# Kernel tuning notes

Measured on AMD Instinct MI355X. Metric: run time of the kernel, lower is better.

Reference implementation:

```python
import jax, jax.numpy as jnp
import numpy as np

N = 10000      # nodes
IN_DIM = 512   # input feature dim
HID = 512      # GCN hidden dim
OUT = 256      # embedding dim
E = 320000     # edges (avg degree 32)


def _normalize(x, eps=1e-12):
    # F.normalize: x / max(||x||_2, eps), row-wise
    n = jnp.sqrt(jnp.sum(x * x, axis=-1, keepdims=True))
    return x / jnp.maximum(n, eps)


def _gcn_conv(x, W, b, src, dst, n):
    # DGL GraphConv with norm='both': D_out^{-1/2} -> sum-aggregate -> D_in^{-1/2}, then bias
    ones = jnp.ones(src.shape[0], x.dtype)
    deg_out = jax.ops.segment_sum(ones, src, num_segments=n)
    deg_in = jax.ops.segment_sum(ones, dst, num_segments=n)
    ns = jnp.where(deg_out > 0, deg_out ** -0.5, 0.0)
    nd = jnp.where(deg_in > 0, deg_in ** -0.5, 0.0)
    h = x @ W                                  # weight first (math-equivalent)
    msg = h[src] * ns[src, None]               # gather + src-normalize
    agg = jax.ops.segment_sum(msg, dst, num_segments=n)  # scatter-sum to dst
    return agg * nd[:, None] + b


def _gcn(x, params, src, dst, n):
    W0, b0, W1, b1 = params
    h = jax.nn.relu(_gcn_conv(x, W0, b0, src, dst, n))
    return _gcn_conv(h, W1, b1, src, dst, n)


def _scores(v, u, Wp, bp, src, dst, n, tau):
    # pos_score: edge sim = <normalize(u)[src], normalize(proj(v))[dst]> / tau, scatter-mean to dst
    q = _normalize(v @ Wp + bp)
    un = _normalize(u)
    sim = jnp.sum(un[src] * q[dst], axis=1) / tau          # [E]
    cnt = jax.ops.segment_sum(jnp.ones_like(sim), dst, num_segments=n)
    denom = jnp.maximum(cnt, 1.0)                          # DGL mean gives 0 for deg-0 nodes
    pos = jax.ops.segment_sum(sim, dst, num_segments=n) / denom
    # neg_score: per-node total similarity (intra + inter), then per-edge log, scatter-mean
    z = _normalize(v)
    stu = _normalize(u)
    neg_sim = jnp.exp(z @ z.T / tau).sum(1) + jnp.exp(z @ stu.T / tau).sum(1)  # [N]
    m = jnp.log(neg_sim[dst] + jnp.exp(sim))               # udf_u_add_log_e
    neg = jax.ops.segment_sum(m, dst, num_segments=n) / denom
    return pos, neg


def setup_inputs() -> dict:
    key = jax.random.key(0)
    ks = jax.random.split(key, 16)
    feat = jax.random.normal(ks[0], (N, IN_DIM), jnp.float32)
    src_g = jax.random.randint(ks[1], (E,), 0, N)
    dst_g = jax.random.randint(ks[2], (E,), 0, N)
    src_s = jax.random.randint(ks[3], (E,), 0, N)
    dst_s = jax.random.randint(ks[4], (E,), 0, N)

    def lin(k, i, o, s=0.05):
        return jax.random.normal(k, (i, o), jnp.float32) * s

    inp = dict(
        feat=feat, src_g=src_g, dst_g=dst_g, src_s=src_s, dst_s=dst_s,
        tau1=jnp.ones((), jnp.float32), tau2=jnp.ones((), jnp.float32),
        # encoder1 (GCN, 2 layers) online + target (deepcopy -> independent params)
        W1a=lin(ks[5], IN_DIM, HID), b1a=jnp.zeros((HID,), jnp.float32),
        W1b=lin(ks[6], HID, OUT), b1b=jnp.zeros((OUT,), jnp.float32),
        W1a_t=lin(ks[7], IN_DIM, HID), b1a_t=jnp.zeros((HID,), jnp.float32),
        W1b_t=lin(ks[8], HID, OUT), b1b_t=jnp.zeros((OUT,), jnp.float32),
        # encoder2 (Linear) online + target
        W2=lin(ks[9], IN_DIM, OUT), b2=jnp.zeros((OUT,), jnp.float32),
        W2_t=lin(ks[10], IN_DIM, OUT), b2_t=jnp.zeros((OUT,), jnp.float32),
        # projector: Predictor(out, out, num_layers=1) -> single Linear
        Wp=lin(ks[11], OUT, OUT), bp=jnp.zeros((OUT,), jnp.float32),
    )
    return inp


def reference(feat, src_g, dst_g, src_s, dst_s, tau1, tau2,
              W1a, b1a, W1b, b1b, W1a_t, b1a_t, W1b_t, b1b_t,
              W2, b2, W2_t, b2_t, Wp, bp):
    n = feat.shape[0]
    # branch 1: GCN encoder
    v1 = _gcn(feat, (W1a, b1a, W1b, b1b), src_g, dst_g, n)
    u1 = _gcn(feat, (W1a_t, b1a_t, W1b_t, b1b_t), src_g, dst_g, n)
    pos1, neg1 = _scores(v1, u1, Wp, bp, src_s, dst_s, n, tau1)
    loss1 = jnp.mean(-pos1 + neg1)
    # branch 2: linear encoder
    v2 = feat @ W2 + b2
    u2 = feat @ W2_t + b2_t
    pos2, neg2 = _scores(v2, u2, Wp, bp, src_s, dst_s, n, tau2)
    loss2 = jnp.mean(-pos2 + neg2)
    return (v1, u1, v2, u2, loss1 + loss2)
```

## Files before the change

kernel.cpp:

```cpp
#include <hip/hip_runtime.h>

typedef __bf16 bf16x8 __attribute__((ext_vector_type(8)));
typedef float f32x4 __attribute__((ext_vector_type(4)));
typedef unsigned short u16x8 __attribute__((ext_vector_type(8)));

#define GLOAD16(gp, lp) __builtin_amdgcn_global_load_lds( \
    (const __attribute__((address_space(1))) void*)(gp), \
    (__attribute__((address_space(3))) void*)(lp), 16, 0, 0)

__device__ __forceinline__ unsigned short f2bf(float f) {
  union { float f; unsigned u; } c; c.f = f;
  unsigned u = c.u;
  u = (u + 0x7fffu + ((u >> 16) & 1u)) >> 16;
  return (unsigned short)u;
}
__device__ __forceinline__ float b2f(unsigned short u) {
  union { unsigned u; float f; } c; c.u = ((unsigned)u) << 16; return c.f;
}

__global__ void k_count(const int* __restrict__ src_g, const int* __restrict__ dst_g,
                        const int* __restrict__ dst_s,
                        int* deg_og, int* deg_ig, int* cnt_s, int E)
{
  int e = blockIdx.x * blockDim.x + threadIdx.x;
  if (e >= E) return;
  atomicAdd(&deg_og[src_g[e]], 1);
  atomicAdd(&deg_ig[dst_g[e]], 1);
  atomicAdd(&cnt_s[dst_s[e]], 1);
}

__global__ void k_norms(const int* __restrict__ deg_og, const int* __restrict__ deg_ig,
                        float* __restrict__ ns, float* __restrict__ nd, int N)
{
  int i = blockIdx.x * blockDim.x + threadIdx.x;
  if (i >= N) return;
  int a = deg_og[i]; ns[i] = a > 0 ? rsqrtf((float)a) : 0.f;
  int b = deg_ig[i]; nd[i] = b > 0 ? rsqrtf((float)b) : 0.f;
}

__global__ __launch_bounds__(1024) void k_scan(const int* __restrict__ deg0, int* __restrict__ offs0,
                                               const int* __restrict__ deg1, int* __restrict__ offs1, int N)
{
  const int* deg = blockIdx.x ? deg1 : deg0;
  int* offs = blockIdx.x ? offs1 : offs0;
  __shared__ int part[1024];
  const int t = threadIdx.x;
  const int CH = (N + 1023) / 1024;
  const int b = t * CH;
  int s = 0;
  for (int i = 0; i < CH; ++i) {
    int idx = b + i;
    s += (idx < N) ? deg[idx] : 0;
  }
  part[t] = s;
  __syncthreads();
  for (int o = 1; o < 1024; o <<= 1) {
    int v = (t >= o) ? part[t - o] : 0;
    __syncthreads();
    part[t] += v;
    __syncthreads();
  }
  int run = (t == 0) ? 0 : part[t - 1];
  if (t == 0) offs[0] = 0;
  for (int i = 0; i < CH; ++i) {
    int idx = b + i;
    if (idx < N) { run += deg[idx]; offs[idx + 1] = run; }
  }
}

__global__ void k_fill(const int* __restrict__ srcA, const int* __restrict__ dstA,
                       const int* __restrict__ offsA, int* curA, int* __restrict__ outA,
                       const int* __restrict__ srcB, const int* __restrict__ dstB,
                       const int* __restrict__ offsB, int* curB, int* __restrict__ outB, int E)
{
  int e = blockIdx.x * blockDim.x + threadIdx.x;
  if (e >= E) return;
  if (blockIdx.y == 0) {
    int d = dstA[e];
    int p = atomicAdd(&curA[d], 1);
    outA[offsA[d] + p] = srcA[e];
  } else {
    int d = dstB[e];
    int p = atomicAdd(&curB[d], 1);
    outB[offsB[d] + p] = srcB[e];
  }
}

struct PrepArgs {
  const float *feat, *W1a, *W1at, *W1b, *W1bt, *W2, *W2t, *Wp;
  const float *b1a, *b1at, *b1b, *b1bt, *b2, *b2t;
  unsigned short *featb, *wcatL1, *wcat2, *wcatLin, *wtp;
  float *bcatL1, *bcatGcn, *bcatLin;
  int NF;
};
__global__ void k_prep(PrepArgs p)
{
  int i = blockIdx.x * blockDim.x + threadIdx.x;
  if (i < p.NF) { p.featb[i] = f2bf(p.feat[i]); return; }
  i -= p.NF;
  if (i < 1024 * 512) {
    int n = i >> 9, k = i & 511;
    p.wcatL1[i] = f2bf(n < 512 ? p.W1a[k * 512 + n] : p.W1at[k * 512 + n - 512]);
    return;
  }
  i -= 1024 * 512;
  if (i < 512 * 512) {
    int n = i >> 9, k = i & 511;
    p.wcat2[i] = f2bf(n < 256 ? p.W1b[k * 256 + n] : p.W1bt[k * 256 + n - 256]);
    return;
  }
  i -= 512 * 512;
  if (i < 512 * 512) {
    int n = i >> 9, k = i & 511;
    p.wcatLin[i] = f2bf(n < 256 ? p.W2[k * 256 + n] : p.W2t[k * 256 + n - 256]);
    return;
  }
  i -= 512 * 512;
  if (i < 256 * 256) {
    int n = i >> 8, k = i & 255;
    p.wtp[i] = f2bf(p.Wp[k * 256 + n]);
    return;
  }
  i -= 256 * 256;
  if (i < 1024) { p.bcatL1[i] = i < 512 ? p.b1a[i] : p.b1at[i - 512]; return; }
  i -= 1024;
  if (i < 512) { p.bcatGcn[i] = i < 256 ? p.b1b[i] : p.b1bt[i - 256]; return; }
  i -= 512;
  if (i < 512) { p.bcatLin[i] = i < 256 ? p.b2[i] : p.b2t[i - 256]; return; }
}

__global__ __launch_bounds__(256) void k_mgemm(
    const unsigned short* __restrict__ A, int lda,
    const unsigned short* __restrict__ Wt,
    const float* __restrict__ bias, float* __restrict__ outf, unsigned short* __restrict__ outb,
    int M, int K, int Nc, int relu, int asel, int splitM)
{
  __shared__ char smem[24576];
  char* As = smem;
  char* Bs = smem + 16384;
  const int tid = threadIdx.x;
  const int lane = tid & 63, w = tid >> 6;
  const int wr = w >> 1, wc = w & 1;
  const int bm = blockIdx.x * 128, bn = blockIdx.y * 64;
  const int aoff = (asel > 0 && bn >= asel) ? K : 0;
  const int srow = lane >> 3;
  const int scol = ((lane & 7) ^ srow) << 3;
  const int xr = (lane & 7) << 4;

  f32x4 acc[4][2];
  #pragma unroll
  for (int mi = 0; mi < 4; ++mi)
    #pragma unroll
    for (int nj = 0; nj < 2; ++nj)
      acc[mi][nj] = (f32x4){0.f, 0.f, 0.f, 0.f};

  for (int k0 = 0; k0 < K; k0 += 64) {
    #pragma unroll
    for (int i = 0; i < 4; ++i) {
      int row = w * 32 + i * 8 + srow;
      int rg = bm + row; rg = rg < M ? rg : M - 1;
      GLOAD16(A + (size_t)rg * lda + aoff + k0 + scol, As + (w * 4096 + i * 1024));
    }
    #pragma unroll
    for (int i = 0; i < 2; ++i) {
      int nrow = w * 16 + i * 8 + srow;
      GLOAD16(Wt + (size_t)(bn + nrow) * K + k0 + scol, Bs + (w * 2048 + i * 1024));
    }
    __syncthreads();
    #pragma unroll
    for (int ks = 0; ks < 2; ++ks) {
      const int kb = ks * 64 + ((lane >> 4) << 4);
      bf16x8 af[4], bfr[2];
      #pragma unroll
      for (int mi = 0; mi < 4; ++mi) {
        int row_l = wr * 64 + mi * 16 + (lane & 15);
        af[mi] = *(const bf16x8*)(As + row_l * 128 + (kb ^ xr));
      }
      #pragma unroll
      for (int nj = 0; nj < 2; ++nj) {
        int n_l = wc * 32 + nj * 16 + (lane & 15);
        bfr[nj] = *(const bf16x8*)(Bs + n_l * 128 + (kb ^ xr));
      }
      __builtin_amdgcn_s_setprio(1);
      #pragma unroll
      for (int mi = 0; mi < 4; ++mi)
        #pragma unroll
        for (int nj = 0; nj < 2; ++nj)
          acc[mi][nj] = __builtin_amdgcn_mfma_f32_16x16x32_bf16(af[mi], bfr[nj], acc[mi][nj], 0, 0, 0);
      __builtin_amdgcn_s_setprio(0);
    }
    __syncthreads();
  }

  #pragma unroll
  for (int mi = 0; mi < 4; ++mi) {
    #pragma unroll
    for (int j = 0; j < 4; ++j) {
      int r = bm + wr * 64 + mi * 16 + ((lane >> 4) << 2) + j;
      if (r >= M) continue;
      #pragma unroll
      for (int nj = 0; nj < 2; ++nj) {
        int c = bn + wc * 32 + nj * 16 + (lane & 15);
        float v = acc[mi][nj][j];
        if (bias) v += bias[c];
        if (relu) v = fmaxf(v, 0.f);
        if (splitM > 0) {
          int rr = r + (c >= 256 ? splitM : 0);
          if (outf) outf[(size_t)rr * 256 + (c & 255)] = v;
          if (outb && c < 256) outb[(size_t)r * 256 + c] = f2bf(v);
        } else {
          if (outf) outf[(size_t)r * Nc + c] = v;
          if (outb) outb[(size_t)r * Nc + c] = f2bf(v);
        }
      }
    }
  }
}

__global__ __launch_bounds__(256) void k_agg(const unsigned short* __restrict__ h,
    const int* __restrict__ offs, const int* __restrict__ csr,
    const float* __restrict__ ns, const float* __restrict__ nd, const float* __restrict__ bias,
    float* __restrict__ outf, unsigned short* __restrict__ outb, int relu, int splitM)
{
  const int node = blockIdx.x * 4 + (threadIdx.x >> 6);
  const int lane = threadIdx.x & 63;
  const int j = lane * 8;
  const int s0 = offs[node], s1 = offs[node + 1];
  float a[8] = {};
  for (int k = s0; k < s1; ++k) {
    const int s = csr[k];
    const float w = ns[s];
    const u16x8 hv = *(const u16x8*)(h + (size_t)s * 512 + j);
    #pragma unroll
    for (int q = 0; q < 8; ++q) a[q] += b2f(hv[q]) * w;
  }
  const float ndv = nd[node];
  float o[8];
  #pragma unroll
  for (int q = 0; q < 8; ++q) {
    o[q] = a[q] * ndv;
    if (bias) o[q] += bias[j + q];
    if (relu) o[q] = fmaxf(o[q], 0.f);
  }
  if (splitM > 0) {
    const int rr = node + (j >= 256 ? splitM : 0);
    const int cc = j & 255;
    if (outf) {
      *(float4*)(outf + (size_t)rr * 256 + cc)     = (float4){o[0], o[1], o[2], o[3]};
      *(float4*)(outf + (size_t)rr * 256 + cc + 4) = (float4){o[4], o[5], o[6], o[7]};
    }
    if (outb && j < 256) {
      u16x8 ub;
      #pragma unroll
      for (int q = 0; q < 8; ++q) ub[q] = f2bf(o[q]);
      *(u16x8*)(outb + (size_t)node * 256 + j) = ub;
    }
  } else {
    if (outf) {
      *(float4*)(outf + (size_t)node * 512 + j)     = (float4){o[0], o[1], o[2], o[3]};
      *(float4*)(outf + (size_t)node * 512 + j + 4) = (float4){o[4], o[5], o[6], o[7]};
    }
    if (outb) {
      u16x8 ub;
      #pragma unroll
      for (int q = 0; q < 8; ++q) ub[q] = f2bf(o[q]);
      *(u16x8*)(outb + (size_t)node * 512 + j) = ub;
    }
  }
}

__global__ __launch_bounds__(256) void k_normrows3(
    const float* __restrict__ X0, unsigned short* __restrict__ O0,
    const float* __restrict__ X1, unsigned short* __restrict__ O1,
    const float* __restrict__ X2, unsigned short* __restrict__ O2, int Nrows)
{
  const float* X = blockIdx.y == 0 ? X0 : (blockIdx.y == 1 ? X1 : X2);
  unsigned short* O = blockIdx.y == 0 ? O0 : (blockIdx.y == 1 ? O1 : O2);
  const int wid = threadIdx.x >> 6, lane = threadIdx.x & 63;
  const int row = blockIdx.x * 4 + wid;
  if (row >= Nrows) return;
  const float4 v = ((const float4*)(X + (size_t)row * 256))[lane];
  float ss = v.x * v.x + v.y * v.y + v.z * v.z + v.w * v.w;
  #pragma unroll
  for (int m = 1; m < 64; m <<= 1) ss += __shfl_xor(ss, m);
  const float inv = 1.f / fmaxf(sqrtf(ss), 1e-12f);
  ushort4 u;
  u.x = f2bf(v.x * inv); u.y = f2bf(v.y * inv);
  u.z = f2bf(v.z * inv); u.w = f2bf(v.w * inv);
  ((ushort4*)(O + (size_t)row * 256))[lane] = u;
}

__global__ __launch_bounds__(256) void k_edge(
    const unsigned short* __restrict__ zun1, const unsigned short* __restrict__ zun2,
    const unsigned short* __restrict__ qb,
    const int* __restrict__ offs_s, const int* __restrict__ csr_es,
    const float* __restrict__ tau1p, const float* __restrict__ tau2p,
    const float* __restrict__ negs1, const float* __restrict__ negs2,
    float* __restrict__ pos1, float* __restrict__ neg1,
    float* __restrict__ pos2, float* __restrict__ neg2, int N)
{
  const int node = blockIdx.x * 4 + (threadIdx.x >> 6);
  if (node >= N) return;
  const int z = blockIdx.y;
  const unsigned short* un = (z ? zun2 : zun1) + (size_t)N * 256;
  const unsigned short* q = qb + (size_t)z * N * 256;
  const float inv_tau = 1.f / (z ? tau2p[0] : tau1p[0]);
  const float nsd = (z ? negs2 : negs1)[node];
  float* pos = z ? pos2 : pos1;
  float* neg = z ? neg2 : neg1;
  const int lane = threadIdx.x & 63;
  const int l = lane & 31, h = lane >> 5;
  const u16x8 qv = *(const u16x8*)(q + (size_t)node * 256 + l * 8);
  float qf[8];
  #pragma unroll
  for (int i = 0; i < 8; ++i) qf[i] = b2f(qv[i]);
  const int s0 = offs_s[node], s1 = offs_s[node + 1];
  float pacc = 0.f, nacc = 0.f;
  for (int k = s0 + h; k < s1; k += 2) {
    const int s = csr_es[k];
    const u16x8 av = *(const u16x8*)(un + (size_t)s * 256 + l * 8);
    float dot = 0.f;
    #pragma unroll
    for (int i = 0; i < 8; ++i) dot += b2f(av[i]) * qf[i];
    #pragma unroll
    for (int m = 1; m < 32; m <<= 1) dot += __shfl_xor(dot, m);
    if (l == 0) {
      const float sv = dot * inv_tau;
      pacc += sv;
      nacc += logf(nsd + __expf(sv));
    }
  }
  pacc += __shfl_xor(pacc, 32);
  nacc += __shfl_xor(nacc, 32);
  if (lane == 0) { pos[node] = pacc; neg[node] = nacc; }
}

#define NEG_JSPLIT 16
#define NEG_TILES 4
__global__ __launch_bounds__(256) void k_negsim(
    const unsigned short* __restrict__ zun1, const unsigned short* __restrict__ zun2,
    const float* __restrict__ tau1p, const float* __restrict__ tau2p,
    float* __restrict__ negs1, float* __restrict__ negs2, int N)
{
  __shared__ char smem[32768];
  const int tid = threadIdx.x;
  const int lane = tid & 63, wid = tid >> 6;
  const int z = blockIdx.z;
  const unsigned short* zun = z ? zun2 : zun1;
  float* negsim = z ? negs2 : negs1;
  const float k_exp = 1.0f / (z ? tau2p[0] : tau1p[0]);
  const int ntiles = N >> 4;
  int itv[NEG_TILES]; bool vv[NEG_TILES];
  #pragma unroll
  for (int t = 0; t < NEG_TILES; ++t) {
    int it = blockIdx.x * (4 * NEG_TILES) + wid * NEG_TILES + t;
    vv[t] = it < ntiles;
    itv[t] = vv[t] ? it : (ntiles - 1);
  }

  bf16x8 afrag[NEG_TILES][8];
  #pragma unroll
  for (int t = 0; t < NEG_TILES; ++t) {
    const unsigned short* r = zun + (size_t)((itv[t] << 4) + (lane & 15)) * 256 + ((lane >> 4) << 3);
    #pragma unroll
    for (int ks = 0; ks < 8; ++ks)
      afrag[t][ks] = *(const bf16x8*)(r + ks * 32);
  }

  const int total = 2 * N;
  const int chunk = ((total + NEG_JSPLIT * 32 - 1) / (NEG_JSPLIT * 32)) * 32;
  const int jbeg = blockIdx.y * chunk;
  const int jend = min(total, jbeg + chunk);
  if (jbeg >= jend) return;

  float psum[NEG_TILES][4];
  #pragma unroll
  for (int t = 0; t < NEG_TILES; ++t)
    #pragma unroll
    for (int j = 0; j < 4; ++j) psum[t][j] = 0.f;

  auto stage = [&](int buf, int j0) {
    #pragma unroll
    for (int i = 0; i < 4; ++i) {
      int idx = tid + 256 * i;
      int r = idx >> 5, c = idx & 31;
      int g = j0 + r; g = g < total ? g : total - 1;
      int cp = c ^ (r & 7);
      GLOAD16(zun + (size_t)g * 256 + cp * 8, smem + buf * 16384 + r * 512 + c * 16);
    }
  };

  const int rxor = (lane & 7) << 4;
  const int kcol = (lane >> 4) << 4;
  int cur = 0;
  stage(0, jbeg);
  if (jbeg + 32 < jend) stage(1, jbeg + 32);
  for (int j0 = jbeg; j0 < jend; j0 += 32) {
    if (j0 + 32 < jend) asm volatile("s_waitcnt vmcnt(4)" ::: "memory");
    else                asm volatile("s_waitcnt vmcnt(0)" ::: "memory");
    __builtin_amdgcn_sched_barrier(0);
    asm volatile("s_barrier" ::: "memory");
    const int rows = min(32, jend - j0);
    const int nsub = rows >> 4;
    const char* base = smem + cur * 16384;
    for (int sub = 0; sub < nsub; ++sub) {
      const char* bb = base + (sub * 16 + (lane & 15)) * 512;
      f32x4 acc[NEG_TILES];
      #pragma unroll
      for (int t = 0; t < NEG_TILES; ++t) acc[t] = (f32x4){0.f, 0.f, 0.f, 0.f};
      __builtin_amdgcn_s_setprio(1);
      #pragma unroll
      for (int ks = 0; ks < 8; ++ks) {
        bf16x8 bfrag = *(const bf16x8*)(bb + ((kcol + ks * 64) ^ rxor));
        #pragma unroll
        for (int t = 0; t < NEG_TILES; ++t)
          acc[t] = __builtin_amdgcn_mfma_f32_16x16x32_bf16(afrag[t][ks], bfrag, acc[t], 0, 0, 0);
      }
      __builtin_amdgcn_s_setprio(0);
      #pragma unroll
      for (int t = 0; t < NEG_TILES; ++t)
        #pragma unroll
        for (int j = 0; j < 4; ++j)
          psum[t][j] += __expf(acc[t][j] * k_exp);
    }
    asm volatile("s_barrier" ::: "memory");
    if (j0 + 64 < jend) stage(cur, j0 + 64);
    cur ^= 1;
  }
  #pragma unroll
  for (int t = 0; t < NEG_TILES; ++t)
    #pragma unroll
    for (int j = 0; j < 4; ++j) {
      float x = psum[t][j];
      x += __shfl_xor(x, 1);
      x += __shfl_xor(x, 2);
      x += __shfl_xor(x, 4);
      x += __shfl_xor(x, 8);
      if (vv[t] && (lane & 15) == 0)
        atomicAdd(&negsim[(itv[t] << 4) + ((lane >> 4) << 2) + j], x);
    }
}

__global__ __launch_bounds__(1024) void k_loss(
    const float* __restrict__ pos1, const float* __restrict__ neg1,
    const float* __restrict__ pos2, const float* __restrict__ neg2,
    const int* __restrict__ cnt, int N, float* __restrict__ out)
{
  __shared__ float lds[1024];
  float s = 0.f;
  for (int i = threadIdx.x; i < N; i += 1024) {
    float denom = fmaxf((float)cnt[i], 1.f);
    s += ((-pos1[i] + neg1[i]) + (-pos2[i] + neg2[i])) / denom;
  }
  lds[threadIdx.x] = s;
  __syncthreads();
  for (int o = 512; o > 0; o >>= 1) {
    if (threadIdx.x < o) lds[threadIdx.x] += lds[threadIdx.x + o];
    __syncthreads();
  }
  if (threadIdx.x == 0) out[0] = lds[0] / (float)N;
}

extern "C" void kernel_launch(void* const* d_in, const int* in_sizes, int n_in,
                              void* d_out, int out_size, void* d_ws, size_t ws_size,
                              hipStream_t stream)
{
  const float* feat  = (const float*)d_in[0];
  const int* src_g   = (const int*)d_in[1];
  const int* dst_g   = (const int*)d_in[2];
  const int* src_s   = (const int*)d_in[3];
  const int* dst_s   = (const int*)d_in[4];
  const float* tau1  = (const float*)d_in[5];
  const float* tau2  = (const float*)d_in[6];
  const float* W1a   = (const float*)d_in[7];
  const float* b1a   = (const float*)d_in[8];
  const float* W1b   = (const float*)d_in[9];
  const float* b1b   = (const float*)d_in[10];
  const float* W1a_t = (const float*)d_in[11];
  const float* b1a_t = (const float*)d_in[12];
  const float* W1b_t = (const float*)d_in[13];
  const float* b1b_t = (const float*)d_in[14];
  const float* W2    = (const float*)d_in[15];
  const float* b2    = (const float*)d_in[16];
  const float* W2_t  = (const float*)d_in[17];
  const float* b2_t  = (const float*)d_in[18];
  const float* Wp    = (const float*)d_in[19];
  const float* bp    = (const float*)d_in[20];

  const int N = in_sizes[0] / 512;
  const int E = in_sizes[1];

  float* out  = (float*)d_out;
  float* v1u1 = out;
  float* v2u2 = out + (size_t)2 * N * 256;
  float* loss = out + (size_t)4 * N * 256;

  char* ws = (char*)d_ws;
  size_t off = 0;
  auto alloc = [&](size_t bytes) -> char* {
    char* p = ws + off;
    off += (bytes + 255) & ~(size_t)255;
    return p;
  };
  int* zbase    = (int*)alloc((size_t)11 * N * 4);
  int* deg_og   = zbase;
  int* deg_ig   = zbase + N;
  int* cnt_s    = zbase + 2 * N;
  int* cursor   = zbase + 3 * N;
  int* cursor_s = zbase + 4 * N;
  float* pos1   = (float*)(zbase + 5 * N);
  float* neg1   = (float*)(zbase + 6 * N);
  float* pos2   = (float*)(zbase + 7 * N);
  float* neg2   = (float*)(zbase + 8 * N);
  float* negs1  = (float*)(zbase + 9 * N);
  float* negs2  = (float*)(zbase + 10 * N);
  int* offs    = (int*)alloc((size_t)(N + 1) * 4);
  int* offs_s  = (int*)alloc((size_t)(N + 1) * 4);
  int* csr_src = (int*)alloc((size_t)E * 4);
  int* csr_es  = (int*)alloc((size_t)E * 4);
  float* ns    = (float*)alloc((size_t)N * 4);
  float* nd    = (float*)alloc((size_t)N * 4);
  unsigned short* featb   = (unsigned short*)alloc((size_t)N * 512 * 2);
  unsigned short* wcatL1  = (unsigned short*)alloc((size_t)1024 * 512 * 2);
  unsigned short* wcat2   = (unsigned short*)alloc((size_t)512 * 512 * 2);
  unsigned short* wcatLin = (unsigned short*)alloc((size_t)512 * 512 * 2);
  unsigned short* wtp     = (unsigned short*)alloc((size_t)256 * 256 * 2);
  float* bcatL1  = (float*)alloc(1024 * 4);
  float* bcatGcn = (float*)alloc(512 * 4);
  float* bcatLin = (float*)alloc(512 * 4);
  char* BUF_H = alloc((size_t)N * 2048);
  char* BUF_A = alloc((size_t)N * 1024);
  char* BUF_B = alloc((size_t)N * 1024);
  char* BUF_C = alloc((size_t)N * 1024);
  char* BUF_E = alloc((size_t)N * 1024);
  if (off > ws_size) return;

  unsigned short* Xaggb = (unsigned short*)BUF_A;
  unsigned short* hcat  = (unsigned short*)BUF_H;
  unsigned short* g2cat = (unsigned short*)BUF_A;
  unsigned short* v1b   = (unsigned short*)BUF_E;
  float*          q_raw = (float*)BUF_H;
  unsigned short* qb    = (unsigned short*)BUF_A;
  unsigned short* zun1  = (unsigned short*)BUF_B;
  unsigned short* zun2  = (unsigned short*)BUF_C;

  const int eb = (E + 255) / 256;
  const int gmx = (N + 127) / 128;
  const int gqx = (2 * N + 127) / 128;
  const int ntiles = N / 16;
  const int ngroups = (ntiles + 4 * NEG_TILES - 1) / (4 * NEG_TILES);
  const dim3 neggrid(ngroups, NEG_JSPLIT, 2);
  const dim3 edgegrid((N + 3) / 4, 2);
  const dim3 nrmgrid((2 * N + 3) / 4, 3);

  hipMemsetAsync(zbase, 0, (size_t)11 * N * 4, stream);
  k_count<<<eb, 256, 0, stream>>>(src_g, dst_g, dst_s, deg_og, deg_ig, cnt_s, E);
  k_norms<<<(N + 255) / 256, 256, 0, stream>>>(deg_og, deg_ig, ns, nd, N);
  k_scan<<<2, 1024, 0, stream>>>(deg_ig, offs, cnt_s, offs_s, N);
  k_fill<<<dim3(eb, 2), 256, 0, stream>>>(src_g, dst_g, offs, cursor, csr_src,
                                          src_s, dst_s, offs_s, cursor_s, csr_es, E);

  PrepArgs pa;
  pa.feat = feat; pa.W1a = W1a; pa.W1at = W1a_t; pa.W1b = W1b; pa.W1bt = W1b_t;
  pa.W2 = W2; pa.W2t = W2_t; pa.Wp = Wp;
  pa.b1a = b1a; pa.b1at = b1a_t; pa.b1b = b1b; pa.b1bt = b1b_t; pa.b2 = b2; pa.b2t = b2_t;
  pa.featb = featb; pa.wcatL1 = wcatL1; pa.wcat2 = wcat2; pa.wcatLin = wcatLin; pa.wtp = wtp;
  pa.bcatL1 = bcatL1; pa.bcatGcn = bcatGcn; pa.bcatLin = bcatLin;
  pa.NF = N * 512;
  const int ptotal = pa.NF + 1024 * 512 + 512 * 512 + 512 * 512 + 256 * 256 + 1024 + 512 + 512;
  k_prep<<<(ptotal + 255) / 256, 256, 0, stream>>>(pa);

  k_agg<<<N / 4, 256, 0, stream>>>(featb, offs, csr_src, ns, nd, nullptr, nullptr, Xaggb, 0, 0);
  k_mgemm<<<dim3(gmx, 16), 256, 0, stream>>>(Xaggb, 512, wcatL1, bcatL1, nullptr, hcat,
                                             N, 512, 1024, 1, 0, 0);
  k_mgemm<<<dim3(gmx, 8), 256, 0, stream>>>(hcat, 1024, wcat2, nullptr, nullptr, g2cat,
                                            N, 512, 512, 0, 256, 0);
  k_agg<<<N / 4, 256, 0, stream>>>(g2cat, offs, csr_src, ns, nd, bcatGcn, v1u1, v1b, 0, N);
  k_mgemm<<<dim3(gmx, 8), 256, 0, stream>>>(featb, 512, wcatLin, bcatLin, v2u2,
                                            (unsigned short*)BUF_E + (size_t)N * 256,
                                            N, 512, 512, 0, 0, N);
  k_mgemm<<<dim3(gqx, 4), 256, 0, stream>>>((unsigned short*)BUF_E, 256, wtp, bp, q_raw, nullptr,
                                            2 * N, 256, 256, 0, 0, 0);

  k_normrows3<<<nrmgrid, 256, 0, stream>>>(v1u1, zun1, v2u2, zun2, q_raw, qb, 2 * N);

  k_negsim<<<neggrid, 256, 0, stream>>>(zun1, zun2, tau1, tau2, negs1, negs2, N);
  k_edge<<<edgegrid, 256, 0, stream>>>(zun1, zun2, qb, offs_s, csr_es, tau1, tau2,
                                       negs1, negs2, pos1, neg1, pos2, neg2, N);
  k_loss<<<1, 1024, 0, stream>>>(pos1, neg1, pos2, neg2, cnt_s, N, loss);
}
```

Measured before the change: 639.0 us.

## Fuse norm kernel into scan, swizzle negsim blocks across XCDs, simplify pipeline

Folds the degree-normalization kernel into the scan launch as extra blocks, which removes one kernel launch. The negsim kernel now uses a flattened 1D grid with an XCD-aware block swizzle, so neighbouring work lands on the same chiplet and L2 reuse should improve. Its prefetch pipeline changes from a two-deep prefetch with manual vmcnt waits to a single-ahead stage with __syncthreads, and exp is computed through exp2f with log2e folded into the scale. The simpler pipeline may hide memory latency less well than the hand-tuned waitcnt version.

```diff
diff --git a/kernel.cpp b/kernel.cpp
--- a/kernel.cpp
+++ b/kernel.cpp
@@ -29,18 +29,19 @@
   atomicAdd(&cnt_s[dst_s[e]], 1);
 }
 
-__global__ void k_norms(const int* __restrict__ deg_og, const int* __restrict__ deg_ig,
-                        float* __restrict__ ns, float* __restrict__ nd, int N)
-{
-  int i = blockIdx.x * blockDim.x + threadIdx.x;
-  if (i >= N) return;
-  int a = deg_og[i]; ns[i] = a > 0 ? rsqrtf((float)a) : 0.f;
-  int b = deg_ig[i]; nd[i] = b > 0 ? rsqrtf((float)b) : 0.f;
-}
-
 __global__ __launch_bounds__(1024) void k_scan(const int* __restrict__ deg0, int* __restrict__ offs0,
-                                               const int* __restrict__ deg1, int* __restrict__ offs1, int N)
-{
+                                               const int* __restrict__ deg1, int* __restrict__ offs1,
+                                               const int* __restrict__ deg_og, const int* __restrict__ deg_ig,
+                                               float* __restrict__ ns, float* __restrict__ nd, int N)
+{
+  if (blockIdx.x >= 2) {
+    int i = (blockIdx.x - 2) * 1024 + threadIdx.x;
+    if (i < N) {
+      int a = deg_og[i]; ns[i] = a > 0 ? rsqrtf((float)a) : 0.f;
+      int b = deg_ig[i]; nd[i] = b > 0 ? rsqrtf((float)b) : 0.f;
+    }
+    return;
+  }
   const int* deg = blockIdx.x ? deg1 : deg0;
   int* offs = blockIdx.x ? offs1 : offs0;
   __shared__ int part[1024];
@@ -340,20 +341,28 @@
 __global__ __launch_bounds__(256) void k_negsim(
     const unsigned short* __restrict__ zun1, const unsigned short* __restrict__ zun2,
     const float* __restrict__ tau1p, const float* __restrict__ tau2p,
-    float* __restrict__ negs1, float* __restrict__ negs2, int N)
+    float* __restrict__ negs1, float* __restrict__ negs2, int N, int ngroups)
 {
   __shared__ char smem[32768];
+  const int nwg = gridDim.x;
+  const int q8 = nwg >> 3, r8 = nwg & 7;
+  const int xcd = blockIdx.x & 7, bidx = blockIdx.x >> 3;
+  const int swz = (xcd < r8 ? xcd * (q8 + 1) : r8 * (q8 + 1) + (xcd - r8) * q8) + bidx;
+  const int bx = swz % ngroups;
+  const int btmp = swz / ngroups;
+  const int by = btmp % NEG_JSPLIT;
+  const int z = btmp / NEG_JSPLIT;
+
   const int tid = threadIdx.x;
   const int lane = tid & 63, wid = tid >> 6;
-  const int z = blockIdx.z;
   const unsigned short* zun = z ? zun2 : zun1;
   float* negsim = z ? negs2 : negs1;
-  const float k_exp = 1.0f / (z ? tau2p[0] : tau1p[0]);
+  const float KE = 1.4426950408889634f / (z ? tau2p[0] : tau1p[0]);
   const int ntiles = N >> 4;
   int itv[NEG_TILES]; bool vv[NEG_TILES];
   #pragma unroll
   for (int t = 0; t < NEG_TILES; ++t) {
-    int it = blockIdx.x * (4 * NEG_TILES) + wid * NEG_TILES + t;
+    int it = bx * (4 * NEG_TILES) + wid * NEG_TILES + t;
     vv[t] = it < ntiles;
     itv[t] = vv[t] ? it : (ntiles - 1);
   }
@@ -369,7 +378,7 @@
 
   const int total = 2 * N;
   const int chunk = ((total + NEG_JSPLIT * 32 - 1) / (NEG_JSPLIT * 32)) * 32;
-  const int jbeg = blockIdx.y * chunk;
+  const int jbeg = by * chunk;
   const int jend = min(total, jbeg + chunk);
   if (jbeg >= jend) return;
 
@@ -394,12 +403,9 @@
   const int kcol = (lane >> 4) << 4;
   int cur = 0;
   stage(0, jbeg);
-  if (jbeg + 32 < jend) stage(1, jbeg + 32);
+  __syncthreads();
   for (int j0 = jbeg; j0 < jend; j0 += 32) {
-    if (j0 + 32 < jend) asm volatile("s_waitcnt vmcnt(4)" ::: "memory");
-    else                asm volatile("s_waitcnt vmcnt(0)" ::: "memory");
-    __builtin_amdgcn_sched_barrier(0);
-    asm volatile("s_barrier" ::: "memory");
+    if (j0 + 32 < jend) stage(cur ^ 1, j0 + 32);
     const int rows = min(32, jend - j0);
     const int nsub = rows >> 4;
     const char* base = smem + cur * 16384;
@@ -421,10 +427,9 @@
       for (int t = 0; t < NEG_TILES; ++t)
         #pragma unroll
         for (int j = 0; j < 4; ++j)
-          psum[t][j] += __expf(acc[t][j] * k_exp);
-    }
-    asm volatile("s_barrier" ::: "memory");
-    if (j0 + 64 < jend) stage(cur, j0 + 64);
+          psum[t][j] += exp2f(acc[t][j] * KE);
+    }
+    __syncthreads();
     cur ^= 1;
   }
   #pragma unroll
@@ -549,14 +554,15 @@
   const int gqx = (2 * N + 127) / 128;
   const int ntiles = N / 16;
   const int ngroups = (ntiles + 4 * NEG_TILES - 1) / (4 * NEG_TILES);
-  const dim3 neggrid(ngroups, NEG_JSPLIT, 2);
+  const int negblocks = ngroups * NEG_JSPLIT * 2;
   const dim3 edgegrid((N + 3) / 4, 2);
   const dim3 nrmgrid((2 * N + 3) / 4, 3);
+  const int scanblocks = 2 + (N + 1023) / 1024;
 
   hipMemsetAsync(zbase, 0, (size_t)11 * N * 4, stream);
   k_count<<<eb, 256, 0, stream>>>(src_g, dst_g, dst_s, deg_og, deg_ig, cnt_s, E);
-  k_norms<<<(N + 255) / 256, 256, 0, stream>>>(deg_og, deg_ig, ns, nd, N);
-  k_scan<<<2, 1024, 0, stream>>>(deg_ig, offs, cnt_s, offs_s, N);
+  k_scan<<<scanblocks, 1024, 0, stream>>>(deg_ig, offs, cnt_s, offs_s,
+                                          deg_og, deg_ig, ns, nd, N);
   k_fill<<<dim3(eb, 2), 256, 0, stream>>>(src_g, dst_g, offs, cursor, csr_src,
                                           src_s, dst_s, offs_s, cursor_s, csr_es, E);
 
@@ -584,7 +590,7 @@
 
   k_normrows3<<<nrmgrid, 256, 0, stream>>>(v1u1, zun1, v2u2, zun2, q_raw, qb, 2 * N);
 
-  k_negsim<<<neggrid, 256, 0, stream>>>(zun1, zun2, tau1, tau2, negs1, negs2, N);
+  k_negsim<<<negblocks, 256, 0, stream>>>(zun1, zun2, tau1, tau2, negs1, negs2, N, ngroups);
   k_edge<<<edgegrid, 256, 0, stream>>>(zun1, zun2, qb, offs_s, csr_es, tau1, tau2,
                                        negs1, negs2, pos1, neg1, pos2, neg2, N);
   k_loss<<<1, 1024, 0, stream>>>(pos1, neg1, pos2, neg2, cnt_s, N, loss);
```

New measurement: 655.9 us. 2.6% more time.
